# Optimization experiments

Hardware: AMD Instinct MI355X
Metric: run time of the kernel (lower is better)

The kernel has to match this reference:

```python
import jax, jax.numpy as jnp
import numpy as np

S = 64            # rendered_size
CLASS_NUM = 14    # dataset.enc_len
NEG_SLOPE = 0.01
EPS = 1e-5


def _conv(x, w, stride, pad):
    return jax.lax.conv_general_dilated(
        x, w, (stride, stride), [(pad, pad), (pad, pad)],
        dimension_numbers=("NCHW", "OIHW", "NCHW"))


def _bn(x, gamma, beta):
    # BatchNorm2d in training mode: biased batch stats over (N,H,W)
    m = jnp.mean(x, axis=(0, 2, 3), keepdims=True)
    v = jnp.var(x, axis=(0, 2, 3), keepdims=True)
    xn = (x - m) * jax.lax.rsqrt(v + EPS)
    return xn * gamma.reshape(1, -1, 1, 1) + beta.reshape(1, -1, 1, 1)


def _lrelu(x):
    return jnp.where(x >= 0, x, NEG_SLOPE * x)


def _render(elements):
    # elements: (B, N, class_num+4)
    rects = elements[:, :, -4:]
    cls = elements[:, :, :-4]                       # (B, N, C)
    x = rects[:, :, 0][:, :, None, None] * S        # (B, N, 1, 1)
    y = rects[:, :, 1][:, :, None, None] * S
    w = rects[:, :, 2][:, :, None, None] * S
    h = rects[:, :, 3][:, :, None, None] * S
    x0, x1 = x - 0.5 * w, x + 0.5 * w
    y0, y1 = y - 0.5 * h, y + 0.5 * h
    cx = jnp.arange(S, dtype=elements.dtype)[None, None, None, :]  # varies along W
    cy = jnp.arange(S, dtype=elements.dtype)[None, None, :, None]  # varies along H
    k = lambda c, cr: jnp.maximum(1.0 - jnp.abs(c - cr), 0.0)
    b0 = lambda c, cr: jnp.clip(c - cr, 0.0, 1.0)
    b1 = lambda cr, c: jnp.clip(cr - c, 0.0, 1.0)
    by = b0(cy, y0) * b1(y1, cy)                    # (B, N, S, S)
    bx = b0(cx, x0) * b1(x1, cx)
    l0 = k(cx, x0) * by
    l1 = k(cx, x1) * by
    l2 = k(cy, y0) * bx
    l3 = k(cy, y1) * bx
    rendered = jnp.maximum(jnp.maximum(l0, l1), jnp.maximum(l2, l3))  # (B,N,S,S)
    # sum over elements of class one-hot * rendered -> (B, C, S, S)
    return jnp.einsum("bnc,bnhw->bchw", cls, rendered)


def setup_inputs() -> dict:
    key = jax.random.key(0)
    ks = jax.random.split(key, 8)
    B, N = 64, 46
    inp = {
        "input_data": jax.random.uniform(ks[0], (B, N, CLASS_NUM + 4), dtype=jnp.float32),
        "input_length": jax.random.randint(ks[1], (B,), 0, N, dtype=jnp.int32),
        # cnn convs (bias=False) + BN affine params
        "w1": jax.random.normal(ks[2], (64, CLASS_NUM, 5, 5), jnp.float32) * 0.05,
        "g1": jnp.ones((64,), jnp.float32), "b1": jnp.zeros((64,), jnp.float32),
        "w2": jax.random.normal(ks[3], (128, 64, 5, 5), jnp.float32) * 0.03,
        "g2": jnp.ones((128,), jnp.float32), "b2": jnp.zeros((128,), jnp.float32),
        "w3": jax.random.normal(ks[4], (256, 128, 5, 5), jnp.float32) * 0.02,
        "g3": jnp.ones((256,), jnp.float32), "b3": jnp.zeros((256,), jnp.float32),
        # classifier: conv k=8 (bias=False) + BN + 1x1 conv (bias=True)
        "w4": jax.random.normal(ks[5], (1024, 256, 8, 8), jnp.float32) * 0.01,
        "g4": jnp.ones((1024,), jnp.float32), "b4": jnp.zeros((1024,), jnp.float32),
        "w5": jax.random.normal(ks[6], (1, 1024, 1, 1), jnp.float32) * 0.03,
        "b5": jnp.zeros((1,), jnp.float32),
    }
    return inp


def reference(input_data, input_length, w1, g1, b1, w2, g2, b2,
              w3, g3, b3, w4, g4, b4, w5, b5):
    rendered = _render(input_data)                       # (B, C, 64, 64)
    h = _lrelu(_bn(_conv(rendered, w1, 2, 2), g1, b1))   # (B, 64, 32, 32)
    h = _lrelu(_bn(_conv(h, w2, 2, 2), g2, b2))          # (B, 128, 16, 16)
    h = _lrelu(_bn(_conv(h, w3, 2, 2), g3, b3))          # (B, 256, 8, 8)
    h = _lrelu(_bn(_conv(h, w4, 1, 0), g4, b4))          # (B, 1024, 1, 1)
    out = _conv(h, w5, 1, 0) + b5.reshape(1, -1, 1, 1)   # (B, 1, 1, 1)
    return out.squeeze()                                 # (B,)
```

## Files before the change

kernel.cpp:

```cpp
#include <hip/hip_runtime.h>
#include <hip/hip_bf16.h>

#define NEG 0.01f
#define EPS 1e-5f

typedef __attribute__((ext_vector_type(8))) short short8;
typedef __attribute__((ext_vector_type(4))) float floatx4;

__device__ inline unsigned short f2bf(float f) {
    __hip_bfloat16 h = __float2bfloat16(f);
    union { __hip_bfloat16 h; unsigned short u; } cv; cv.h = h;
    return cv.u;
}

__global__ __launch_bounds__(256) void render_kernel(const float* __restrict__ in,
                                                     unsigned short* __restrict__ out) {
    int b = blockIdx.x >> 4;
    int chunk = blockIdx.x & 15;
    __shared__ float r0[46], r1[46], r2[46], r3[46];
    __shared__ float cls_s[46 * 14];
    int tid = threadIdx.x;
    if (tid < 46) {
        const float* p = in + ((size_t)b * 46 + tid) * 18 + 14;
        float x = p[0] * 64.f, y = p[1] * 64.f, w = p[2] * 64.f, h = p[3] * 64.f;
        r0[tid] = x - 0.5f * w; r1[tid] = x + 0.5f * w;
        r2[tid] = y - 0.5f * h; r3[tid] = y + 0.5f * h;
    }
    for (int idx = tid; idx < 46 * 14; idx += 256) {
        int n = idx / 14, c = idx % 14;
        cls_s[idx] = in[((size_t)b * 46 + n) * 18 + c];
    }
    __syncthreads();
    if (tid < 33) {
        int j = chunk * 33 + tid;
        if (j < 528) {
            int y, x;
            if (j < 136) { y = j / 68; x = j - y * 68; }
            else if (j < 272) { int t = j - 136; int yy = t / 68; y = 66 + yy; x = t - yy * 68; }
            else { int t = j - 272; y = 2 + (t >> 2); int k = t & 3; x = (k < 2) ? k : 64 + k; }
            size_t zb = (((size_t)b * 68 + y) * 68 + x) * 16;
            short8 z;
#pragma unroll
            for (int i = 0; i < 8; ++i) z[i] = 0;
            *(short8*)(out + zb) = z;
            *(short8*)(out + zb + 8) = z;
        }
    }
    int pix = chunk * 256 + tid;
    float cx = (float)(pix & 63);
    float cy = (float)(pix >> 6);
    float acc[14];
#pragma unroll
    for (int c = 0; c < 14; ++c) acc[c] = 0.f;
    for (int n = 0; n < 46; ++n) {
        float x0 = r0[n], x1 = r1[n], y0 = r2[n], y1 = r3[n];
        float by = fminf(fmaxf(cy - y0, 0.f), 1.f) * fminf(fmaxf(y1 - cy, 0.f), 1.f);
        float bx = fminf(fmaxf(cx - x0, 0.f), 1.f) * fminf(fmaxf(x1 - cx, 0.f), 1.f);
        float kx0 = fmaxf(1.f - fabsf(cx - x0), 0.f);
        float kx1 = fmaxf(1.f - fabsf(cx - x1), 0.f);
        float ky0 = fmaxf(1.f - fabsf(cy - y0), 0.f);
        float ky1 = fmaxf(1.f - fabsf(cy - y1), 0.f);
        float r = fmaxf(fmaxf(kx0 * by, kx1 * by), fmaxf(ky0 * bx, ky1 * bx));
        if (r > 0.f) {
#pragma unroll
            for (int c = 0; c < 14; ++c) acc[c] = fmaf(cls_s[n * 14 + c], r, acc[c]);
        }
    }
    size_t obase = (((size_t)b * 68 + ((pix >> 6) + 2)) * 68 + ((pix & 63) + 2)) * 16;
    short8 v0, v1;
#pragma unroll
    for (int i = 0; i < 8; ++i) v0[i] = (short)f2bf(acc[i]);
#pragma unroll
    for (int i = 0; i < 6; ++i) v1[i] = (short)f2bf(acc[8 + i]);
    v1[6] = 0; v1[7] = 0;
    *(short8*)(out + obase) = v0;
    *(short8*)(out + obase + 8) = v1;
}

__global__ __launch_bounds__(256) void wtrans_all(const float* __restrict__ w1,
                                                  const float* __restrict__ w2,
                                                  const float* __restrict__ w3,
                                                  unsigned short* __restrict__ wT1,
                                                  unsigned short* __restrict__ wT2,
                                                  unsigned short* __restrict__ wT3) {
    int idx = blockIdx.x * 256 + threadIdx.x;
    const float* w; unsigned short* wT; int CIN, CPLOG, SUB, COLOG;
    if (idx < 30720) { w = w1; wT = wT1; CIN = 14; CPLOG = 4; SUB = 3; COLOG = 6; }
    else if (idx < 235520) { idx -= 30720; w = w2; wT = wT2; CIN = 64; CPLOG = 6; SUB = 10; COLOG = 7; }
    else if (idx < 1054720) { idx -= 235520; w = w3; wT = wT3; CIN = 128; CPLOG = 7; SUB = 20; COLOG = 8; }
    else return;
    int kk = idx & 31;
    int co = (idx >> 5) & ((1 << COLOG) - 1);
    int s = idx >> (5 + COLOG);
    int kh = s / SUB, sub = s - kh * SUB;
    int kidx = sub * 32 + kk;
    int kw = kidx >> CPLOG;
    int ci = kidx & ((1 << CPLOG) - 1);
    float v = (kw < 5 && ci < CIN) ? w[((size_t)(co * CIN + ci) * 5 + kh) * 5 + kw] : 0.f;
    wT[idx] = f2bf(v);
}

template <int CP, int COUT, int HP, int LOG_OHW, int LOG_OW, int SUB,
          int NCO, int NT, int CH, int NW>
__global__ __launch_bounds__(NW * 64) void conv_mfma(
        const unsigned short* __restrict__ inP,
        const unsigned short* __restrict__ wT,
        float* __restrict__ outX,
        float* __restrict__ stacc) {
    constexpr int NSTEP = 5 * SUB;
    constexpr int NCHUNK = NSTEP / CH;
    constexpr int COT = NT * 16;
    constexpr int NSTG = (CH * COT * 4) / (NW * 64);
    static_assert(NSTEP % CH == 0, "CH must divide NSTEP");
    static_assert((CH * COT * 4) % (NW * 64) == 0, "staging must tile evenly");
    __shared__ short Bs[2][CH][COT][32];
    __shared__ float sred[NW][2][COT];
    int tid = threadIdx.x;
    int wave = tid >> 6, lane = tid & 63, q = lane >> 4, l16 = lane & 15;
    int bm = blockIdx.x / NCO, bco = blockIdx.x % NCO;

    const short* aB[4];
#pragma unroll
    for (int f = 0; f < 4; ++f) {
        int m = bm * (NW * 64) + wave * 64 + f * 16 + l16;
        int b = m >> LOG_OHW;
        int ohw = m & ((1 << LOG_OHW) - 1);
        int oh = ohw >> LOG_OW, ow = ohw & ((1 << LOG_OW) - 1);
        aB[f] = (const short*)inP + ((size_t)((b * HP + 2 * oh) * HP + 2 * ow)) * CP + q * 8;
    }
    const short* bgbase = (const short*)wT + (size_t)bco * COT * 32;

    floatx4 acc[4][NT];
#pragma unroll
    for (int f = 0; f < 4; ++f)
#pragma unroll
        for (int nt = 0; nt < NT; ++nt) acc[f][nt] = (floatx4){0.f, 0.f, 0.f, 0.f};

    short8 nb[NSTG];
#pragma unroll
    for (int i = 0; i < NSTG; ++i) {
        int v = tid + i * NW * 64;
        int s = v / (COT * 4);
        int rem = v - s * (COT * 4);
        nb[i] = *(const short8*)(bgbase + ((size_t)s * COUT) * 32 + rem * 8);
    }
#pragma unroll
    for (int i = 0; i < NSTG; ++i) {
        int v = tid + i * NW * 64;
        int s = v / (COT * 4);
        int rem = v - s * (COT * 4);
        *(short8*)((short*)&Bs[0][s][0][0] + rem * 8) = nb[i];
    }
    __syncthreads();

    for (int chunk = 0; chunk < NCHUNK; ++chunk) {
        int cur = chunk & 1;
        if (chunk + 1 < NCHUNK) {
            int step0 = (chunk + 1) * CH;
#pragma unroll
            for (int i = 0; i < NSTG; ++i) {
                int v = tid + i * NW * 64;
                int s = v / (COT * 4);
                int rem = v - s * (COT * 4);
                nb[i] = *(const short8*)(bgbase + ((size_t)(step0 + s) * COUT) * 32 + rem * 8);
            }
        }
#pragma unroll
        for (int s = 0; s < CH; ++s) {
            int step = chunk * CH + s;
            int kh = step / SUB, sub = step - kh * SUB;
            short8 af[4];
#pragma unroll
            for (int f = 0; f < 4; ++f)
                af[f] = *(const short8*)(aB[f] + (size_t)(kh * HP) * CP + sub * 32);
#pragma unroll
            for (int nt = 0; nt < NT; ++nt) {
                short8 bf = *(const short8*)&Bs[cur][s][nt * 16 + l16][q * 8];
#pragma unroll
                for (int f = 0; f < 4; ++f)
                    acc[f][nt] = __builtin_amdgcn_mfma_f32_16x16x32_bf16(af[f], bf, acc[f][nt], 0, 0, 0);
            }
        }
        if (chunk + 1 < NCHUNK) {
#pragma unroll
            for (int i = 0; i < NSTG; ++i) {
                int v = tid + i * NW * 64;
                int s = v / (COT * 4);
                int rem = v - s * (COT * 4);
                *(short8*)((short*)&Bs[cur ^ 1][s][0][0] + rem * 8) = nb[i];
            }
            __syncthreads();
        }
    }
#pragma unroll
    for (int f = 0; f < 4; ++f)
#pragma unroll
        for (int nt = 0; nt < NT; ++nt)
#pragma unroll
            for (int rg = 0; rg < 4; ++rg) {
                int mg = bm * (NW * 64) + wave * 64 + f * 16 + q * 4 + rg;
                int co = bco * COT + nt * 16 + l16;
                outX[(size_t)mg * COUT + co] = acc[f][nt][rg];
            }
#pragma unroll
    for (int nt = 0; nt < NT; ++nt) {
        float s = 0.f, s2 = 0.f;
#pragma unroll
        for (int f = 0; f < 4; ++f)
#pragma unroll
            for (int rg = 0; rg < 4; ++rg) {
                float v = acc[f][nt][rg];
                s += v; s2 = fmaf(v, v, s2);
            }
        s += __shfl_xor(s, 16); s += __shfl_xor(s, 32);
        s2 += __shfl_xor(s2, 16); s2 += __shfl_xor(s2, 32);
        if (q == 0) {
            sred[wave][0][nt * 16 + l16] = s;
            sred[wave][1][nt * 16 + l16] = s2;
        }
    }
    __syncthreads();
    if (tid < COT) {
        float ts = 0.f, ts2 = 0.f;
#pragma unroll
        for (int w = 0; w < NW; ++w) { ts += sred[w][0][tid]; ts2 += sred[w][1][tid]; }
        atomicAdd(&stacc[bco * COT + tid], ts);
        atomicAdd(&stacc[COUT + bco * COT + tid], ts2);
    }
}

__global__ __launch_bounds__(256) void conv4_mfma(const unsigned short* __restrict__ A,
                                                  const float* __restrict__ w4,
                                                  float* __restrict__ h4) {
    constexpr int CH = 4, NCHUNK = 8;
    __shared__ short Bs[CH][64][40];
    int tid = threadIdx.x;
    int bco = blockIdx.x & 15;
    int ks = blockIdx.x >> 4;
    int wave = tid >> 6, lane = tid & 63, q = lane >> 4, l16 = lane & 15;
    const short* aBase = (const short*)A + (size_t)(wave * 16 + l16) * 16384 + ks * 1024 + q * 8;
    int r = tid >> 2, cc = tid & 3;
    const float* bg = w4 + (size_t)(bco * 64 + r) * 16384 + ks * 1024 + cc * 8;

    floatx4 acc[4];
#pragma unroll
    for (int nt = 0; nt < 4; ++nt) acc[nt] = (floatx4){0.f, 0.f, 0.f, 0.f};

    short8 nb[CH];
#pragma unroll
    for (int s = 0; s < CH; ++s) {
        float4 b0 = *(const float4*)(bg + s * 32);
        float4 b1 = *(const float4*)(bg + s * 32 + 4);
        nb[s][0] = (short)f2bf(b0.x); nb[s][1] = (short)f2bf(b0.y);
        nb[s][2] = (short)f2bf(b0.z); nb[s][3] = (short)f2bf(b0.w);
        nb[s][4] = (short)f2bf(b1.x); nb[s][5] = (short)f2bf(b1.y);
        nb[s][6] = (short)f2bf(b1.z); nb[s][7] = (short)f2bf(b1.w);
    }
#pragma unroll
    for (int s = 0; s < CH; ++s) *(short8*)&Bs[s][r][cc * 8] = nb[s];
    __syncthreads();

    for (int chunk = 0; chunk < NCHUNK; ++chunk) {
        bool has_next = (chunk + 1 < NCHUNK);
        if (has_next) {
#pragma unroll
            for (int s = 0; s < CH; ++s) {
                int step = (chunk + 1) * CH + s;
                float4 b0 = *(const float4*)(bg + step * 32);
                float4 b1 = *(const float4*)(bg + step * 32 + 4);
                nb[s][0] = (short)f2bf(b0.x); nb[s][1] = (short)f2bf(b0.y);
                nb[s][2] = (short)f2bf(b0.z); nb[s][3] = (short)f2bf(b0.w);
                nb[s][4] = (short)f2bf(b1.x); nb[s][5] = (short)f2bf(b1.y);
                nb[s][6] = (short)f2bf(b1.z); nb[s][7] = (short)f2bf(b1.w);
            }
        }
#pragma unroll
        for (int s = 0; s < CH; ++s) {
            int step = chunk * CH + s;
            short8 af = *(const short8*)(aBase + step * 32);
#pragma unroll
            for (int nt = 0; nt < 4; ++nt) {
                short8 bf = *(const short8*)&Bs[s][nt * 16 + l16][q * 8];
                acc[nt] = __builtin_amdgcn_mfma_f32_16x16x32_bf16(af, bf, acc[nt], 0, 0, 0);
            }
        }
        if (has_next) {
            __syncthreads();
#pragma unroll
            for (int s = 0; s < CH; ++s) *(short8*)&Bs[s][r][cc * 8] = nb[s];
            __syncthreads();
        }
    }
#pragma unroll
    for (int nt = 0; nt < 4; ++nt) {
#pragma unroll
        for (int rg = 0; rg < 4; ++rg) {
            int mg = wave * 16 + q * 4 + rg;
            int co = bco * 64 + nt * 16 + l16;
            atomicAdd(&h4[(size_t)mg * 1024 + co], acc[nt][rg]);
        }
    }
}

__global__ __launch_bounds__(256) void stats_part(const float* __restrict__ X,
                                                  float* __restrict__ acc,
                                                  int CO, int R, int RPB, int CGLOG) {
    int tid = threadIdx.x;
    int cg = blockIdx.x & ((1 << CGLOG) - 1);
    int rb = blockIdx.x >> CGLOG;
    int c = (cg << 6) + (tid & 63);
    int w = tid >> 6;
    float s = 0.f, s2 = 0.f;
    int rend = min(R, (rb + 1) * RPB);
    for (int r = rb * RPB + w; r < rend; r += 4) {
        float v = X[(size_t)r * CO + c];
        s += v; s2 += v * v;
    }
    __shared__ float ls[4][64], ls2[4][64];
    ls[w][tid & 63] = s; ls2[w][tid & 63] = s2;
    __syncthreads();
    if (tid < 64) {
        float ts = ls[0][tid] + ls[1][tid] + ls[2][tid] + ls[3][tid];
        float ts2 = ls2[0][tid] + ls2[1][tid] + ls2[2][tid] + ls2[3][tid];
        int cc = (cg << 6) + tid;
        atomicAdd(&acc[cc], ts);
        atomicAdd(&acc[CO + cc], ts2);
    }
}

__global__ __launch_bounds__(256) void bnpad_kernel(const float* __restrict__ X,
                                                    const float* __restrict__ stacc,
                                                    const float* __restrict__ g,
                                                    const float* __restrict__ bb,
                                                    unsigned short* __restrict__ out,
                                                    int CO_LOG, int OH, int OHP,
                                                    float invN, int total) {
    int idx = blockIdx.x * 256 + threadIdx.x;
    if (idx >= total) return;
    int CO = 1 << CO_LOG;
    int c = idx & (CO - 1);
    float mean = stacc[c] * invN;
    float var = fmaxf(stacc[CO + c] * invN - mean * mean, 0.f);
    float sc = g[c] * rsqrtf(var + EPS);
    float sh = bb[c] - mean * sc;
    int t = idx >> CO_LOG;
    int x = t % OHP; t /= OHP;
    int y = t % OHP; int b = t / OHP;
    unsigned short v = 0;
    if (y >= 2 && y < OH + 2 && x >= 2 && x < OH + 2) {
        float f = X[(((size_t)(b * OH + (y - 2)) * OH + (x - 2)) << CO_LOG) + c];
        f = f * sc + sh;
        f = f >= 0.f ? f : NEG * f;
        v = f2bf(f);
    }
    out[idx] = v;
}

__global__ __launch_bounds__(256) void bn_nchw_kernel(const float* __restrict__ X,
                                                      const float* __restrict__ stacc,
                                                      const float* __restrict__ g,
                                                      const float* __restrict__ bb,
                                                      unsigned short* __restrict__ out,
                                                      int total) {
    int idx = blockIdx.x * 256 + threadIdx.x;
    if (idx >= total) return;
    int hw = idx & 63;
    int ci = (idx >> 6) & 255;
    int b = idx >> 14;
    float mean = stacc[ci] * (1.f / 4096.f);
    float var = fmaxf(stacc[256 + ci] * (1.f / 4096.f) - mean * mean, 0.f);
    float sc = g[ci] * rsqrtf(var + EPS);
    float sh = bb[ci] - mean * sc;
    float f = X[((size_t)(b * 64 + hw)) * 256 + ci] * sc + sh;
    f = f >= 0.f ? f : NEG * f;
    out[idx] = f2bf(f);
}

__global__ __launch_bounds__(256) void conv5_kernel(const float* __restrict__ X,
                                                    const float* __restrict__ stacc,
                                                    const float* __restrict__ g,
                                                    const float* __restrict__ bb,
                                                    const float* __restrict__ w5,
                                                    const float* __restrict__ b5,
                                                    float* __restrict__ out) {
    int b = blockIdx.x, tid = threadIdx.x;
    float s = 0.f;
    for (int c = tid; c < 1024; c += 256) {
        float mean = stacc[c] * (1.f / 64.f);
        float var = fmaxf(stacc[1024 + c] * (1.f / 64.f) - mean * mean, 0.f);
        float sc = g[c] * rsqrtf(var + EPS);
        float sh = bb[c] - mean * sc;
        float f = X[(size_t)b * 1024 + c] * sc + sh;
        f = f >= 0.f ? f : NEG * f;
        s = fmaf(f, w5[c], s);
    }
#pragma unroll
    for (int off = 32; off > 0; off >>= 1) s += __shfl_down(s, off);
    __shared__ float ls[4];
    if ((tid & 63) == 0) ls[tid >> 6] = s;
    __syncthreads();
    if (tid == 0) out[b] = ls[0] + ls[1] + ls[2] + ls[3] + b5[0];
}

extern "C" void kernel_launch(void* const* d_in, const int* in_sizes, int n_in,
                              void* d_out, int out_size, void* d_ws, size_t ws_size,
                              hipStream_t stream) {
    (void)in_sizes; (void)n_in; (void)out_size; (void)ws_size;
    const float* input_data = (const float*)d_in[0];
    const float* w1 = (const float*)d_in[2];
    const float* g1 = (const float*)d_in[3];
    const float* b1 = (const float*)d_in[4];
    const float* w2 = (const float*)d_in[5];
    const float* g2 = (const float*)d_in[6];
    const float* b2 = (const float*)d_in[7];
    const float* w3 = (const float*)d_in[8];
    const float* g3 = (const float*)d_in[9];
    const float* b3 = (const float*)d_in[10];
    const float* w4 = (const float*)d_in[11];
    const float* g4 = (const float*)d_in[12];
    const float* b4 = (const float*)d_in[13];
    const float* w5 = (const float*)d_in[14];
    const float* b5 = (const float*)d_in[15];

    char* ws = (char*)d_ws;
    float* regA = (float*)ws;
    char* wsB = ws + 16777216;
    char* wsC = wsB + 10616832;
    char* wsD = wsC + 9469952;
    float* h4  = (float*)wsD;
    float* st1 = (float*)(wsD + 262144);
    float* st2 = (float*)(wsD + 262656);
    float* st3 = (float*)(wsD + 263680);
    float* st4 = (float*)(wsD + 265728);
    unsigned short* wT1 = (unsigned short*)(wsD + 274432);
    unsigned short* wT2 = (unsigned short*)(wsD + 335872);
    unsigned short* wT3 = (unsigned short*)(wsD + 745472);

    unsigned short* rendered = (unsigned short*)wsC;
    float* conv1out = regA;
    unsigned short* pad1 = (unsigned short*)wsB;
    float* conv2out = (float*)wsC;
    unsigned short* pad2 = (unsigned short*)wsB;
    float* conv3out = regA;
    unsigned short* a4 = (unsigned short*)wsC;

    hipMemsetAsync(wsD, 0, 273920, stream);
    wtrans_all<<<4120, 256, 0, stream>>>(w1, w2, w3, wT1, wT2, wT3);
    render_kernel<<<1024, 256, 0, stream>>>(input_data, rendered);

    conv_mfma<16, 64, 68, 10, 5, 3, 1, 4, 5, 4><<<256, 256, 0, stream>>>(rendered, wT1, conv1out, st1);
    bnpad_kernel<<<20736, 256, 0, stream>>>(conv1out, st1, g1, b1, pad1, 6, 32, 36, 1.f / 65536.f, 5308416);

    conv_mfma<64, 128, 36, 8, 4, 10, 4, 2, 10, 4><<<256, 256, 0, stream>>>(pad1, wT2, conv2out, st2);
    bnpad_kernel<<<12800, 256, 0, stream>>>(conv2out, st2, g2, b2, pad2, 7, 16, 20, 1.f / 16384.f, 3276800);

    conv_mfma<128, 256, 20, 6, 3, 20, 8, 2, 10, 2><<<256, 128, 0, stream>>>(pad2, wT3, conv3out, st3);
    bn_nchw_kernel<<<4096, 256, 0, stream>>>(conv3out, st3, g3, b3, a4, 1048576);

    conv4_mfma<<<256, 256, 0, stream>>>(a4, w4, h4);
    stats_part<<<16, 256, 0, stream>>>(h4, st4, 1024, 64, 64, 4);

    conv5_kernel<<<64, 256, 0, stream>>>(h4, st4, g4, b4, w5, b5, (float*)d_out);
}
```

Before: 280.5 us.

## Fuse render with weight transform; direct-load convs with split-K and XCD swizzle

Merges the weight-transpose kernel into the render kernel so a single launch does both. Replaces the LDS-staged, double-buffered conv kernel with one that loads A and B fragments straight from global memory into registers with one-step prefetch. The new kernel uses an XCD-aware block remap and 512 blocks with 2 blocks per SM for occupancy. Conv3 is split along K into 4 segments that combine results with atomicAdd into a zeroed buffer, so a separate stats pass is now needed. Conv4's staging chunk is enlarged. The cost is atomic traffic, a larger memset and an extra kernel.

```diff
diff --git a/kernel.cpp b/kernel.cpp
--- a/kernel.cpp
+++ b/kernel.cpp
@@ -13,12 +13,36 @@
     return cv.u;
 }
 
-__global__ __launch_bounds__(256) void render_kernel(const float* __restrict__ in,
-                                                     unsigned short* __restrict__ out) {
+__global__ __launch_bounds__(256) void head_kernel(const float* __restrict__ in,
+                                                   unsigned short* __restrict__ out,
+                                                   const float* __restrict__ w1,
+                                                   const float* __restrict__ w2,
+                                                   const float* __restrict__ w3,
+                                                   unsigned short* __restrict__ wT1,
+                                                   unsigned short* __restrict__ wT2,
+                                                   unsigned short* __restrict__ wT3) {
+    __shared__ float r0[46], r1[46], r2[46], r3[46];
+    __shared__ float cls_s[46 * 14];
+    if (blockIdx.x >= 1024) {
+        int idx = (blockIdx.x - 1024) * 256 + threadIdx.x;
+        const float* w; unsigned short* wT; int CIN, CPLOG, SUB, COLOG;
+        if (idx < 30720) { w = w1; wT = wT1; CIN = 14; CPLOG = 4; SUB = 3; COLOG = 6; }
+        else if (idx < 235520) { idx -= 30720; w = w2; wT = wT2; CIN = 64; CPLOG = 6; SUB = 10; COLOG = 7; }
+        else if (idx < 1054720) { idx -= 235520; w = w3; wT = wT3; CIN = 128; CPLOG = 7; SUB = 20; COLOG = 8; }
+        else return;
+        int kk = idx & 31;
+        int co = (idx >> 5) & ((1 << COLOG) - 1);
+        int s = idx >> (5 + COLOG);
+        int kh = s / SUB, sub = s - kh * SUB;
+        int kidx = sub * 32 + kk;
+        int kw = kidx >> CPLOG;
+        int ci = kidx & ((1 << CPLOG) - 1);
+        float v = (kw < 5 && ci < CIN) ? w[((size_t)(co * CIN + ci) * 5 + kh) * 5 + kw] : 0.f;
+        wT[idx] = f2bf(v);
+        return;
+    }
     int b = blockIdx.x >> 4;
     int chunk = blockIdx.x & 15;
-    __shared__ float r0[46], r1[46], r2[46], r3[46];
-    __shared__ float cls_s[46 * 14];
     int tid = threadIdx.x;
     if (tid < 46) {
         const float* p = in + ((size_t)b * 46 + tid) * 18 + 14;
@@ -77,58 +101,41 @@
     *(short8*)(out + obase + 8) = v1;
 }
 
-__global__ __launch_bounds__(256) void wtrans_all(const float* __restrict__ w1,
-                                                  const float* __restrict__ w2,
-                                                  const float* __restrict__ w3,
-                                                  unsigned short* __restrict__ wT1,
-                                                  unsigned short* __restrict__ wT2,
-                                                  unsigned short* __restrict__ wT3) {
-    int idx = blockIdx.x * 256 + threadIdx.x;
-    const float* w; unsigned short* wT; int CIN, CPLOG, SUB, COLOG;
-    if (idx < 30720) { w = w1; wT = wT1; CIN = 14; CPLOG = 4; SUB = 3; COLOG = 6; }
-    else if (idx < 235520) { idx -= 30720; w = w2; wT = wT2; CIN = 64; CPLOG = 6; SUB = 10; COLOG = 7; }
-    else if (idx < 1054720) { idx -= 235520; w = w3; wT = wT3; CIN = 128; CPLOG = 7; SUB = 20; COLOG = 8; }
-    else return;
-    int kk = idx & 31;
-    int co = (idx >> 5) & ((1 << COLOG) - 1);
-    int s = idx >> (5 + COLOG);
-    int kh = s / SUB, sub = s - kh * SUB;
-    int kidx = sub * 32 + kk;
-    int kw = kidx >> CPLOG;
-    int ci = kidx & ((1 << CPLOG) - 1);
-    float v = (kw < 5 && ci < CIN) ? w[((size_t)(co * CIN + ci) * 5 + kh) * 5 + kw] : 0.f;
-    wT[idx] = f2bf(v);
-}
-
 template <int CP, int COUT, int HP, int LOG_OHW, int LOG_OW, int SUB,
-          int NCO, int NT, int CH, int NW>
-__global__ __launch_bounds__(NW * 64) void conv_mfma(
+          int NCO, int NT, int KSEG>
+__global__ __launch_bounds__(256, 2) void conv_direct(
         const unsigned short* __restrict__ inP,
         const unsigned short* __restrict__ wT,
         float* __restrict__ outX,
         float* __restrict__ stacc) {
-    constexpr int NSTEP = 5 * SUB;
-    constexpr int NCHUNK = NSTEP / CH;
+    constexpr int NSTEP_TOT = 5 * SUB;
+    constexpr int NSTEP = NSTEP_TOT / KSEG;
     constexpr int COT = NT * 16;
-    constexpr int NSTG = (CH * COT * 4) / (NW * 64);
-    static_assert(NSTEP % CH == 0, "CH must divide NSTEP");
-    static_assert((CH * COT * 4) % (NW * 64) == 0, "staging must tile evenly");
-    __shared__ short Bs[2][CH][COT][32];
-    __shared__ float sred[NW][2][COT];
+    static_assert(NSTEP_TOT % KSEG == 0, "KSEG must divide steps");
+    __shared__ float sred[4][2][COT];
     int tid = threadIdx.x;
     int wave = tid >> 6, lane = tid & 63, q = lane >> 4, l16 = lane & 15;
-    int bm = blockIdx.x / NCO, bco = blockIdx.x % NCO;
+    int cpx = gridDim.x >> 3;
+    int lb = (blockIdx.x & 7) * cpx + (blockIdx.x >> 3);
+    int bm = lb / (NCO * KSEG);
+    int rem = lb - bm * (NCO * KSEG);
+    int bco = rem / KSEG;
+    int kseg = rem - bco * KSEG;
+    int kbase = kseg * NSTEP;
 
     const short* aB[4];
 #pragma unroll
     for (int f = 0; f < 4; ++f) {
-        int m = bm * (NW * 64) + wave * 64 + f * 16 + l16;
+        int m = bm * 256 + wave * 64 + f * 16 + l16;
         int b = m >> LOG_OHW;
         int ohw = m & ((1 << LOG_OHW) - 1);
         int oh = ohw >> LOG_OW, ow = ohw & ((1 << LOG_OW) - 1);
         aB[f] = (const short*)inP + ((size_t)((b * HP + 2 * oh) * HP + 2 * ow)) * CP + q * 8;
     }
-    const short* bgbase = (const short*)wT + (size_t)bco * COT * 32;
+    const short* bB[NT];
+#pragma unroll
+    for (int nt = 0; nt < NT; ++nt)
+        bB[nt] = (const short*)wT + (size_t)bco * COT * 32 + ((nt * 16 + l16) * 4 + q) * 8;
 
     floatx4 acc[4][NT];
 #pragma unroll
@@ -136,103 +143,87 @@
 #pragma unroll
         for (int nt = 0; nt < NT; ++nt) acc[f][nt] = (floatx4){0.f, 0.f, 0.f, 0.f};
 
-    short8 nb[NSTG];
-#pragma unroll
-    for (int i = 0; i < NSTG; ++i) {
-        int v = tid + i * NW * 64;
-        int s = v / (COT * 4);
-        int rem = v - s * (COT * 4);
-        nb[i] = *(const short8*)(bgbase + ((size_t)s * COUT) * 32 + rem * 8);
-    }
-#pragma unroll
-    for (int i = 0; i < NSTG; ++i) {
-        int v = tid + i * NW * 64;
-        int s = v / (COT * 4);
-        int rem = v - s * (COT * 4);
-        *(short8*)((short*)&Bs[0][s][0][0] + rem * 8) = nb[i];
-    }
-    __syncthreads();
-
-    for (int chunk = 0; chunk < NCHUNK; ++chunk) {
-        int cur = chunk & 1;
-        if (chunk + 1 < NCHUNK) {
-            int step0 = (chunk + 1) * CH;
-#pragma unroll
-            for (int i = 0; i < NSTG; ++i) {
-                int v = tid + i * NW * 64;
-                int s = v / (COT * 4);
-                int rem = v - s * (COT * 4);
-                nb[i] = *(const short8*)(bgbase + ((size_t)(step0 + s) * COUT) * 32 + rem * 8);
+    short8 afc[4], bfc[NT], afn[4], bfn[NT];
+    {
+        int gs = kbase;
+        int kh = gs / SUB, sub = gs - kh * SUB;
+#pragma unroll
+        for (int f = 0; f < 4; ++f)
+            afc[f] = *(const short8*)(aB[f] + (size_t)kh * HP * CP + sub * 32);
+#pragma unroll
+        for (int nt = 0; nt < NT; ++nt)
+            bfc[nt] = *(const short8*)(bB[nt] + (size_t)gs * COUT * 32);
+    }
+#pragma unroll
+    for (int s = 0; s < NSTEP; ++s) {
+        if (s + 1 < NSTEP) {
+            int gs = kbase + s + 1;
+            int kh = gs / SUB, sub = gs - kh * SUB;
+#pragma unroll
+            for (int f = 0; f < 4; ++f)
+                afn[f] = *(const short8*)(aB[f] + (size_t)kh * HP * CP + sub * 32);
+#pragma unroll
+            for (int nt = 0; nt < NT; ++nt)
+                bfn[nt] = *(const short8*)(bB[nt] + (size_t)gs * COUT * 32);
+        }
+#pragma unroll
+        for (int nt = 0; nt < NT; ++nt)
+#pragma unroll
+            for (int f = 0; f < 4; ++f)
+                acc[f][nt] = __builtin_amdgcn_mfma_f32_16x16x32_bf16(afc[f], bfc[nt], acc[f][nt], 0, 0, 0);
+        if (s + 1 < NSTEP) {
+#pragma unroll
+            for (int f = 0; f < 4; ++f) afc[f] = afn[f];
+#pragma unroll
+            for (int nt = 0; nt < NT; ++nt) bfc[nt] = bfn[nt];
+        }
+    }
+#pragma unroll
+    for (int f = 0; f < 4; ++f)
+#pragma unroll
+        for (int nt = 0; nt < NT; ++nt)
+#pragma unroll
+            for (int rg = 0; rg < 4; ++rg) {
+                int mg = bm * 256 + wave * 64 + f * 16 + q * 4 + rg;
+                int co = bco * COT + nt * 16 + l16;
+                if constexpr (KSEG > 1)
+                    atomicAdd(&outX[(size_t)mg * COUT + co], acc[f][nt][rg]);
+                else
+                    outX[(size_t)mg * COUT + co] = acc[f][nt][rg];
             }
-        }
-#pragma unroll
-        for (int s = 0; s < CH; ++s) {
-            int step = chunk * CH + s;
-            int kh = step / SUB, sub = step - kh * SUB;
-            short8 af[4];
+    if constexpr (KSEG == 1) {
+#pragma unroll
+        for (int nt = 0; nt < NT; ++nt) {
+            float s = 0.f, s2 = 0.f;
 #pragma unroll
             for (int f = 0; f < 4; ++f)
-                af[f] = *(const short8*)(aB[f] + (size_t)(kh * HP) * CP + sub * 32);
-#pragma unroll
-            for (int nt = 0; nt < NT; ++nt) {
-                short8 bf = *(const short8*)&Bs[cur][s][nt * 16 + l16][q * 8];
-#pragma unroll
-                for (int f = 0; f < 4; ++f)
-                    acc[f][nt] = __builtin_amdgcn_mfma_f32_16x16x32_bf16(af[f], bf, acc[f][nt], 0, 0, 0);
+#pragma unroll
+                for (int rg = 0; rg < 4; ++rg) {
+                    float v = acc[f][nt][rg];
+                    s += v; s2 = fmaf(v, v, s2);
+                }
+            s += __shfl_xor(s, 16); s += __shfl_xor(s, 32);
+            s2 += __shfl_xor(s2, 16); s2 += __shfl_xor(s2, 32);
+            if (q == 0) {
+                sred[wave][0][nt * 16 + l16] = s;
+                sred[wave][1][nt * 16 + l16] = s2;
             }
         }
-        if (chunk + 1 < NCHUNK) {
-#pragma unroll
-            for (int i = 0; i < NSTG; ++i) {
-                int v = tid + i * NW * 64;
-                int s = v / (COT * 4);
-                int rem = v - s * (COT * 4);
-                *(short8*)((short*)&Bs[cur ^ 1][s][0][0] + rem * 8) = nb[i];
-            }
-            __syncthreads();
-        }
-    }
-#pragma unroll
-    for (int f = 0; f < 4; ++f)
-#pragma unroll
-        for (int nt = 0; nt < NT; ++nt)
-#pragma unroll
-            for (int rg = 0; rg < 4; ++rg) {
-                int mg = bm * (NW * 64) + wave * 64 + f * 16 + q * 4 + rg;
-                int co = bco * COT + nt * 16 + l16;
-                outX[(size_t)mg * COUT + co] = acc[f][nt][rg];
-            }
-#pragma unroll
-    for (int nt = 0; nt < NT; ++nt) {
-        float s = 0.f, s2 = 0.f;
-#pragma unroll
-        for (int f = 0; f < 4; ++f)
-#pragma unroll
-            for (int rg = 0; rg < 4; ++rg) {
-                float v = acc[f][nt][rg];
-                s += v; s2 = fmaf(v, v, s2);
-            }
-        s += __shfl_xor(s, 16); s += __shfl_xor(s, 32);
-        s2 += __shfl_xor(s2, 16); s2 += __shfl_xor(s2, 32);
-        if (q == 0) {
-            sred[wave][0][nt * 16 + l16] = s;
-            sred[wave][1][nt * 16 + l16] = s2;
-        }
-    }
-    __syncthreads();
-    if (tid < COT) {
-        float ts = 0.f, ts2 = 0.f;
-#pragma unroll
-        for (int w = 0; w < NW; ++w) { ts += sred[w][0][tid]; ts2 += sred[w][1][tid]; }
-        atomicAdd(&stacc[bco * COT + tid], ts);
-        atomicAdd(&stacc[COUT + bco * COT + tid], ts2);
+        __syncthreads();
+        if (tid < COT) {
+            float ts = 0.f, ts2 = 0.f;
+#pragma unroll
+            for (int w = 0; w < 4; ++w) { ts += sred[w][0][tid]; ts2 += sred[w][1][tid]; }
+            atomicAdd(&stacc[bco * COT + tid], ts);
+            atomicAdd(&stacc[COUT + bco * COT + tid], ts2);
+        }
     }
 }
 
 __global__ __launch_bounds__(256) void conv4_mfma(const unsigned short* __restrict__ A,
                                                   const float* __restrict__ w4,
                                                   float* __restrict__ h4) {
-    constexpr int CH = 4, NCHUNK = 8;
+    constexpr int CH = 8, NCHUNK = 4;
     __shared__ short Bs[CH][64][40];
     int tid = threadIdx.x;
     int bco = blockIdx.x & 15;
@@ -432,29 +423,29 @@
     float* st2 = (float*)(wsD + 262656);
     float* st3 = (float*)(wsD + 263680);
     float* st4 = (float*)(wsD + 265728);
-    unsigned short* wT1 = (unsigned short*)(wsD + 274432);
-    unsigned short* wT2 = (unsigned short*)(wsD + 335872);
-    unsigned short* wT3 = (unsigned short*)(wsD + 745472);
+    float* conv3out = (float*)(wsD + 274432);
+    unsigned short* wT1 = (unsigned short*)(wsD + 4468736);
+    unsigned short* wT2 = (unsigned short*)(wsD + 4530176);
+    unsigned short* wT3 = (unsigned short*)(wsD + 4939776);
 
     unsigned short* rendered = (unsigned short*)wsC;
     float* conv1out = regA;
     unsigned short* pad1 = (unsigned short*)wsB;
     float* conv2out = (float*)wsC;
     unsigned short* pad2 = (unsigned short*)wsB;
-    float* conv3out = regA;
     unsigned short* a4 = (unsigned short*)wsC;
 
-    hipMemsetAsync(wsD, 0, 273920, stream);
-    wtrans_all<<<4120, 256, 0, stream>>>(w1, w2, w3, wT1, wT2, wT3);
-    render_kernel<<<1024, 256, 0, stream>>>(input_data, rendered);
-
-    conv_mfma<16, 64, 68, 10, 5, 3, 1, 4, 5, 4><<<256, 256, 0, stream>>>(rendered, wT1, conv1out, st1);
+    hipMemsetAsync(wsD, 0, 4468736, stream);
+    head_kernel<<<5144, 256, 0, stream>>>(input_data, rendered, w1, w2, w3, wT1, wT2, wT3);
+
+    conv_direct<16, 64, 68, 10, 5, 3, 2, 2, 1><<<512, 256, 0, stream>>>(rendered, wT1, conv1out, st1);
     bnpad_kernel<<<20736, 256, 0, stream>>>(conv1out, st1, g1, b1, pad1, 6, 32, 36, 1.f / 65536.f, 5308416);
 
-    conv_mfma<64, 128, 36, 8, 4, 10, 4, 2, 10, 4><<<256, 256, 0, stream>>>(pad1, wT2, conv2out, st2);
+    conv_direct<64, 128, 36, 8, 4, 10, 8, 1, 1><<<512, 256, 0, stream>>>(pad1, wT2, conv2out, st2);
     bnpad_kernel<<<12800, 256, 0, stream>>>(conv2out, st2, g2, b2, pad2, 7, 16, 20, 1.f / 16384.f, 3276800);
 
-    conv_mfma<128, 256, 20, 6, 3, 20, 8, 2, 10, 2><<<256, 128, 0, stream>>>(pad2, wT3, conv3out, st3);
+    conv_direct<128, 256, 20, 6, 3, 20, 8, 2, 4><<<512, 256, 0, stream>>>(pad2, wT3, conv3out, st3);
+    stats_part<<<256, 256, 0, stream>>>(conv3out, st3, 256, 4096, 64, 2);
     bn_nchw_kernel<<<4096, 256, 0, stream>>>(conv3out, st3, g3, b3, a4, 1048576);
 
     conv4_mfma<<<256, 256, 0, stream>>>(a4, w4, h4);
```

New measurement: 323.3 us. 1.15x slower.
